# Optimization experiments

Hardware: AMD Instinct MI355X
Metric: run time of the kernel (lower is better)

## Reference

```python
import jax, jax.numpy as jnp
import numpy as np

HID = 24

def setup_inputs() -> dict:
    key = jax.random.key(0)
    ks = jax.random.split(key, 20)
    B, T = 1024, 4096
    s = 0.1
    inp = {
        "x": jax.random.normal(ks[0], (B, T, 1), jnp.float32),
        "h": jnp.zeros((3, B, HID), jnp.float32),
        # RNN layer 0 (input size 1)
        "W_ih0": jax.random.normal(ks[1], (HID, 1), jnp.float32) * s,
        "b_ih0": jax.random.normal(ks[2], (HID,), jnp.float32) * s,
        "W_hh0": jax.random.normal(ks[3], (HID, HID), jnp.float32) * s,
        "b_hh0": jax.random.normal(ks[4], (HID,), jnp.float32) * s,
        # RNN layer 1
        "W_ih1": jax.random.normal(ks[5], (HID, HID), jnp.float32) * s,
        "b_ih1": jax.random.normal(ks[6], (HID,), jnp.float32) * s,
        "W_hh1": jax.random.normal(ks[7], (HID, HID), jnp.float32) * s,
        "b_hh1": jax.random.normal(ks[8], (HID,), jnp.float32) * s,
        # RNN layer 2
        "W_ih2": jax.random.normal(ks[9], (HID, HID), jnp.float32) * s,
        "b_ih2": jax.random.normal(ks[10], (HID,), jnp.float32) * s,
        "W_hh2": jax.random.normal(ks[11], (HID, HID), jnp.float32) * s,
        "b_hh2": jax.random.normal(ks[12], (HID,), jnp.float32) * s,
        # MLP head 24 -> 24 -> 1
        "W1": jax.random.normal(ks[13], (HID, HID), jnp.float32) * s,
        "b1": jax.random.normal(ks[14], (HID,), jnp.float32) * s,
        "W2": jax.random.normal(ks[15], (1, HID), jnp.float32) * s,
        "b2": jax.random.normal(ks[16], (1,), jnp.float32) * s,
    }
    return inp


def reference(x, h,
              W_ih0, b_ih0, W_hh0, b_hh0,
              W_ih1, b_ih1, W_hh1, b_hh1,
              W_ih2, b_ih2, W_hh2, b_hh2,
              W1, b1, W2, b2):
    # x: [B, T, 1]; h: [3, B, 24]. force=True -> every step uses x[:, i, :];
    # returned y is the MLP output of the LAST timestep only.
    relu = jax.nn.relu

    def cell(carry, x_t):  # x_t: [B, 1]
        h0, h1, h2 = carry
        h0n = relu(x_t @ W_ih0.T + b_ih0 + h0 @ W_hh0.T + b_hh0)
        h1n = relu(h0n @ W_ih1.T + b_ih1 + h1 @ W_hh1.T + b_hh1)
        h2n = relu(h1n @ W_ih2.T + b_ih2 + h2 @ W_hh2.T + b_hh2)
        y = relu(relu(h2n @ W1.T + b1) @ W2.T + b2)  # [B, 1]
        return (h0n, h1n, h2n), y

    xs = jnp.swapaxes(x, 0, 1)  # [T, B, 1]
    (h0f, h1f, h2f), ys = jax.lax.scan(cell, (h[0], h[1], h[2]), xs)
    y = ys[-1]                       # [B, 1]
    h_final = jnp.stack([h0f, h1f, h2f])  # [3, B, 24]
    return y, h_final
```

## Files before the change

kernel.cpp:

```cpp
#include <hip/hip_runtime.h>

#define HID   24
#define T_LEN 4096
#define BATCH 1024
#define NB    2
#define K     32
#define NC    (T_LEN / K)
#define CTOT  (NC + 2)
#define TPB   192
#define PS    32

typedef __attribute__((ext_vector_type(2))) _Float16 h2v;
typedef __attribute__((ext_vector_type(4))) int      int4v;

#if __has_builtin(__builtin_amdgcn_fdot2)
__device__ __forceinline__ float dot2f(int p, int w, float acc) {
    return __builtin_amdgcn_fdot2(__builtin_bit_cast(h2v, p),
                                  __builtin_bit_cast(h2v, w), acc, false);
}
#else
__device__ __forceinline__ float dot2f(int p, int w, float acc) {
    h2v a = __builtin_bit_cast(h2v, p), b = __builtin_bit_cast(h2v, w);
    acc = fmaf((float)a.x, (float)b.x, acc);
    return fmaf((float)a.y, (float)b.y, acc);
}
#endif

__device__ __forceinline__ float dot4(const float4 a, const float4 b, float acc) {
    acc = fmaf(a.x, b.x, acc);
    acc = fmaf(a.y, b.y, acc);
    acc = fmaf(a.z, b.z, acc);
    return fmaf(a.w, b.w, acc);
}

#define PKF(A_, B_)                                                                 \
    (((int)__builtin_bit_cast(unsigned short, (_Float16)(B_)) << 16) |              \
     (int)__builtin_bit_cast(unsigned short, (_Float16)(A_)))

__global__ __launch_bounds__(TPB, 1) void rnn_ra_kernel(
    const float* __restrict__ x,
    const float* __restrict__ h_in,
    const float* __restrict__ Wih0, const float* __restrict__ bih0,
    const float* __restrict__ Whh0, const float* __restrict__ bhh0,
    const float* __restrict__ Wih1, const float* __restrict__ bih1,
    const float* __restrict__ Whh1, const float* __restrict__ bhh1,
    const float* __restrict__ Wih2, const float* __restrict__ bih2,
    const float* __restrict__ Whh2, const float* __restrict__ bhh2,
    const float* __restrict__ W1,   const float* __restrict__ b1,
    const float* __restrict__ W2,   const float* __restrict__ b2,
    float* __restrict__ out)
{
    __shared__ __align__(16) _Float16 row0[2][NB][PS];
    __shared__ __align__(16) _Float16 row2[2][NB][PS];
    __shared__ __align__(16) _Float16 pub1[2][NB][K][PS];
    __shared__ __align__(16) float part1[2][NB][K][PS];
    __shared__ float h2f[NB][HID];
    __shared__ float mbuf[NB][HID];

    const int tid  = threadIdx.x;
    const int l    = tid >> 6;
    const int lane = tid & 63;
    const int bl   = lane >> 5;
    const int jj   = lane & 31;
    const bool act = (jj < HID);
    const int uL   = act ? jj : (jj - 8);
    const int bg   = blockIdx.x * NB + bl;

    int4v whA, whB, whC;
    int4v wiA = {0,0,0,0}, wiB = {0,0,0,0}, wiC = {0,0,0,0};
    float wx0 = 0.f, bias;

#define MK3(ROW, DA, DB, DC) do {                                                   \
        DA = (int4v){PKF((ROW)[0], (ROW)[1]),   PKF((ROW)[2], (ROW)[3]),            \
                     PKF((ROW)[4], (ROW)[5]),   PKF((ROW)[6], (ROW)[7])};           \
        DB = (int4v){PKF((ROW)[8], (ROW)[9]),   PKF((ROW)[10], (ROW)[11]),          \
                     PKF((ROW)[12], (ROW)[13]), PKF((ROW)[14], (ROW)[15])};         \
        DC = (int4v){PKF((ROW)[16], (ROW)[17]), PKF((ROW)[18], (ROW)[19]),          \
                     PKF((ROW)[20], (ROW)[21]), PKF((ROW)[22], (ROW)[23])};         \
    } while (0)

    if (l == 0) {
        MK3(Whh0 + uL * HID, whA, whB, whC);
        MK3(Wih1 + uL * HID, wiA, wiB, wiC);
        wx0  = Wih0[uL];
        bias = bih0[uL] + bhh0[uL];
    } else if (l == 1) {
        MK3(Whh1 + uL * HID, whA, whB, whC);
        bias = bih1[uL] + bhh1[uL];
    } else {
        MK3(Whh2 + uL * HID, whA, whB, whC);
        MK3(Wih2 + uL * HID, wiA, wiB, wiC);
        bias = bih2[uL] + bhh2[uL];
    }
#undef MK3

    float cur = h_in[(l * BATCH + bg) * HID + uL];

    int4v o0, o1, o2;
    if (l == 0) {
        row0[1][bl][jj] = (_Float16)cur;
        const int4v* r = (const int4v*)&row0[1][bl][0];
        o0 = r[0]; o1 = r[1]; o2 = r[2];
    } else if (l == 1) {
        pub1[0][bl][K - 1][jj] = (_Float16)cur;
        const int4v* r = (const int4v*)&pub1[0][bl][K - 1][0];
        o0 = r[0]; o1 = r[1]; o2 = r[2];
    } else {
        row2[1][bl][jj] = (_Float16)cur;
        const int4v* r = (const int4v*)&row2[1][bl][0];
        o0 = r[0]; o1 = r[1]; o2 = r[2];
    }

    const float* xrow = x + (size_t)bg * T_LEN;
    float4 xq[8], xn[8];
    if (l == 0) {
        const float4* xr = (const float4*)xrow;
        #pragma unroll
        for (int q = 0; q < 8; ++q) xq[q] = xr[q];
    }
#define XV(S)                                                                       \
    (((S) & 3) == 0 ? xq[(S) >> 2].x : ((S) & 3) == 1 ? xq[(S) >> 2].y              \
   : ((S) & 3) == 2 ? xq[(S) >> 2].z : xq[(S) >> 2].w)

#define DOT12(V0_, V1_, V2_, W0_, W1_, W2_, A0_, A1_)                               \
    A0_ = dot2f(V0_.x, W0_.x, A0_); A1_ = dot2f(V0_.y, W0_.y, A1_);                 \
    A0_ = dot2f(V0_.z, W0_.z, A0_); A1_ = dot2f(V0_.w, W0_.w, A1_);                 \
    A0_ = dot2f(V1_.x, W1_.x, A0_); A1_ = dot2f(V1_.y, W1_.y, A1_);                 \
    A0_ = dot2f(V1_.z, W1_.z, A0_); A1_ = dot2f(V1_.w, W1_.w, A1_);                 \
    A0_ = dot2f(V2_.x, W2_.x, A0_); A1_ = dot2f(V2_.y, W2_.y, A1_);                 \
    A0_ = dot2f(V2_.z, W2_.z, A0_); A1_ = dot2f(V2_.w, W2_.w, A1_);

    __syncthreads();

    for (int c = 0; c < CTOT; ++c) {
        const int wp = c & 1, rp = wp ^ 1;
        if (l == 0) {
            if (c < NC) {
                const bool pf = (c + 1 < NC);
                if (pf) {
                    const float4* xr = (const float4*)(xrow + (size_t)(c + 1) * K);
                    #pragma unroll
                    for (int q = 0; q < 8; ++q) xn[q] = xr[q];
                }
                float* dst = &part1[wp][bl][0][0];
                #pragma unroll
                for (int s = 0; s < K; ++s) {
                    float a0 = fmaf(wx0, XV(s), bias), a1 = 0.f;
                    DOT12(o0, o1, o2, whA, whB, whC, a0, a1);
                    cur = fmaxf(a0 + a1, 0.f);
                    row0[s & 1][bl][jj] = (_Float16)cur;
                    const int4v* r = (const int4v*)&row0[s & 1][bl][0];
                    const int4v n0 = r[0], n1 = r[1], n2 = r[2];
                    if (s > 0) {
                        float p0 = 0.f, p1 = 0.f;
                        DOT12(o0, o1, o2, wiA, wiB, wiC, p0, p1);
                        dst[(s - 1) * PS + jj] = p0 + p1;
                    }
                    o0 = n0; o1 = n1; o2 = n2;
                }
                {
                    float p0 = 0.f, p1 = 0.f;
                    DOT12(o0, o1, o2, wiA, wiB, wiC, p0, p1);
                    dst[(K - 1) * PS + jj] = p0 + p1;
                }
                if (pf) {
                    #pragma unroll
                    for (int q = 0; q < 8; ++q) xq[q] = xn[q];
                }
            }
        } else if (l == 1) {
            if (c >= 1 && c < 1 + NC) {
                const float* srcp = &part1[rp][bl][0][0];
                #pragma unroll
                for (int s = 0; s < K; ++s) {
                    const float pin = srcp[s * PS + jj];
                    float a0 = pin + bias, a1 = 0.f;
                    DOT12(o0, o1, o2, whA, whB, whC, a0, a1);
                    cur = fmaxf(a0 + a1, 0.f);
                    pub1[wp][bl][s][jj] = (_Float16)cur;
                    const int4v* r = (const int4v*)&pub1[wp][bl][s][0];
                    o0 = r[0]; o1 = r[1]; o2 = r[2];
                }
            }
        } else {
            if (c >= 2 && c < 2 + NC) {
                const int4v* src = (const int4v*)&pub1[rp][bl][0][0];
                int4v iA0 = src[0], iA1 = src[1], iA2 = src[2];
                #pragma unroll
                for (int s = 0; s < K; ++s) {
                    float a0 = bias, a1 = 0.f, a2 = 0.f, a3 = 0.f;
                    DOT12(iA0, iA1, iA2, wiA, wiB, wiC, a0, a1);
                    DOT12(o0, o1, o2, whA, whB, whC, a2, a3);
                    cur = fmaxf((a0 + a1) + (a2 + a3), 0.f);
                    row2[s & 1][bl][jj] = (_Float16)cur;
                    const int4v* r = (const int4v*)&row2[s & 1][bl][0];
                    const int4v n0 = r[0], n1 = r[1], n2 = r[2];
                    if (s + 1 < K) {
                        const int4v* nr = (const int4v*)&pub1[rp][bl][s + 1][0];
                        iA0 = nr[0]; iA1 = nr[1]; iA2 = nr[2];
                    }
                    o0 = n0; o1 = n1; o2 = n2;
                }
            }
        }
        __syncthreads();
    }
#undef XV
#undef DOT12

    if (act) out[BATCH + (size_t)(l * BATCH + bg) * HID + uL] = cur;

    if (l == 2 && act) h2f[bl][uL] = cur;
    __syncthreads();
    if (l == 2 && act) {
        const float4* w1r = (const float4*)(W1 + uL * HID);
        const float4* hv  = (const float4*)&h2f[bl][0];
        float a = b1[uL];
        a = dot4(w1r[0], hv[0], a); a = dot4(w1r[1], hv[1], a);
        a = dot4(w1r[2], hv[2], a); a = dot4(w1r[3], hv[3], a);
        a = dot4(w1r[4], hv[4], a); a = dot4(w1r[5], hv[5], a);
        mbuf[bl][uL] = fmaxf(a, 0.f);
    }
    __syncthreads();
    if (l == 2 && jj == 0) {
        float a = b2[0];
        #pragma unroll
        for (int k = 0; k < HID; ++k) a = fmaf(W2[k], mbuf[bl][k], a);
        out[bg] = fmaxf(a, 0.f);
    }
}

extern "C" void kernel_launch(void* const* d_in, const int* in_sizes, int n_in,
                              void* d_out, int out_size, void* d_ws, size_t ws_size,
                              hipStream_t stream) {
    const float* x    = (const float*)d_in[0];
    const float* h_in = (const float*)d_in[1];
    const float* Wih0 = (const float*)d_in[2];
    const float* bih0 = (const float*)d_in[3];
    const float* Whh0 = (const float*)d_in[4];
    const float* bhh0 = (const float*)d_in[5];
    const float* Wih1 = (const float*)d_in[6];
    const float* bih1 = (const float*)d_in[7];
    const float* Whh1 = (const float*)d_in[8];
    const float* bhh1 = (const float*)d_in[9];
    const float* Wih2 = (const float*)d_in[10];
    const float* bih2 = (const float*)d_in[11];
    const float* Whh2 = (const float*)d_in[12];
    const float* bhh2 = (const float*)d_in[13];
    const float* W1   = (const float*)d_in[14];
    const float* b1   = (const float*)d_in[15];
    const float* W2   = (const float*)d_in[16];
    const float* b2   = (const float*)d_in[17];
    float* out = (float*)d_out;

    dim3 grid(BATCH / NB);
    dim3 block(TPB);
    hipLaunchKernelGGL(rnn_ra_kernel, grid, block, 0, stream,
                       x, h_in, Wih0, bih0, Whh0, bhh0,
                       Wih1, bih1, Whh1, bhh1, Wih2, bih2, Whh2, bhh2,
                       W1, b1, W2, b2, out);
}
```

Baseline: 510.1 us.

## Move layer-2 input projection into layer-1 wave with lagged partial sums

Layer 1's wave now computes the W_ih2 projection of its own outputs, one step behind, and writes fp32 partial sums into a new part2 buffer. Layer 2's wave then runs only its recurrent dot product plus a preloaded partial, matching how layer 0 already feeds layer 1. This balances the per-step work across the three pipelined waves and shortens layer 2's serial dependency chain. In exchange it adds shared memory for part2 and row1, and lengthens layer 1's per-step work.

```diff
diff --git a/kernel.cpp b/kernel.cpp
--- a/kernel.cpp
+++ b/kernel.cpp
@@ -37,7 +37,7 @@
     (((int)__builtin_bit_cast(unsigned short, (_Float16)(B_)) << 16) |              \
      (int)__builtin_bit_cast(unsigned short, (_Float16)(A_)))
 
-__global__ __launch_bounds__(TPB, 1) void rnn_ra_kernel(
+__global__ __launch_bounds__(TPB, 1) void rnn_lag_kernel(
     const float* __restrict__ x,
     const float* __restrict__ h_in,
     const float* __restrict__ Wih0, const float* __restrict__ bih0,
@@ -51,9 +51,10 @@
     float* __restrict__ out)
 {
     __shared__ __align__(16) _Float16 row0[2][NB][PS];
+    __shared__ __align__(16) _Float16 row1[2][NB][PS];
     __shared__ __align__(16) _Float16 row2[2][NB][PS];
-    __shared__ __align__(16) _Float16 pub1[2][NB][K][PS];
     __shared__ __align__(16) float part1[2][NB][K][PS];
+    __shared__ __align__(16) float part2[2][NB][K][PS];
     __shared__ float h2f[NB][HID];
     __shared__ float mbuf[NB][HID];
 
@@ -86,10 +87,10 @@
         bias = bih0[uL] + bhh0[uL];
     } else if (l == 1) {
         MK3(Whh1 + uL * HID, whA, whB, whC);
+        MK3(Wih2 + uL * HID, wiA, wiB, wiC);
         bias = bih1[uL] + bhh1[uL];
     } else {
         MK3(Whh2 + uL * HID, whA, whB, whC);
-        MK3(Wih2 + uL * HID, wiA, wiB, wiC);
         bias = bih2[uL] + bhh2[uL];
     }
 #undef MK3
@@ -102,8 +103,8 @@
         const int4v* r = (const int4v*)&row0[1][bl][0];
         o0 = r[0]; o1 = r[1]; o2 = r[2];
     } else if (l == 1) {
-        pub1[0][bl][K - 1][jj] = (_Float16)cur;
-        const int4v* r = (const int4v*)&pub1[0][bl][K - 1][0];
+        row1[1][bl][jj] = (_Float16)cur;
+        const int4v* r = (const int4v*)&row1[1][bl][0];
         o0 = r[0]; o1 = r[1]; o2 = r[2];
     } else {
         row2[1][bl][jj] = (_Float16)cur;
@@ -171,35 +172,41 @@
         } else if (l == 1) {
             if (c >= 1 && c < 1 + NC) {
                 const float* srcp = &part1[rp][bl][0][0];
+                float* dstp = &part2[wp][bl][0][0];
                 #pragma unroll
                 for (int s = 0; s < K; ++s) {
                     const float pin = srcp[s * PS + jj];
                     float a0 = pin + bias, a1 = 0.f;
                     DOT12(o0, o1, o2, whA, whB, whC, a0, a1);
                     cur = fmaxf(a0 + a1, 0.f);
-                    pub1[wp][bl][s][jj] = (_Float16)cur;
-                    const int4v* r = (const int4v*)&pub1[wp][bl][s][0];
-                    o0 = r[0]; o1 = r[1]; o2 = r[2];
+                    row1[s & 1][bl][jj] = (_Float16)cur;
+                    const int4v* r = (const int4v*)&row1[s & 1][bl][0];
+                    const int4v n0 = r[0], n1 = r[1], n2 = r[2];
+                    if (s > 0) {
+                        float p0 = 0.f, p1 = 0.f;
+                        DOT12(o0, o1, o2, wiA, wiB, wiC, p0, p1);
+                        dstp[(s - 1) * PS + jj] = p0 + p1;
+                    }
+                    o0 = n0; o1 = n1; o2 = n2;
+                }
+                {
+                    float p0 = 0.f, p1 = 0.f;
+                    DOT12(o0, o1, o2, wiA, wiB, wiC, p0, p1);
+                    dstp[(K - 1) * PS + jj] = p0 + p1;
                 }
             }
         } else {
             if (c >= 2 && c < 2 + NC) {
-                const int4v* src = (const int4v*)&pub1[rp][bl][0][0];
-                int4v iA0 = src[0], iA1 = src[1], iA2 = src[2];
+                const float* srcp = &part2[rp][bl][0][0];
                 #pragma unroll
                 for (int s = 0; s < K; ++s) {
-                    float a0 = bias, a1 = 0.f, a2 = 0.f, a3 = 0.f;
-                    DOT12(iA0, iA1, iA2, wiA, wiB, wiC, a0, a1);
-                    DOT12(o0, o1, o2, whA, whB, whC, a2, a3);
-                    cur = fmaxf((a0 + a1) + (a2 + a3), 0.f);
+                    const float pin = srcp[s * PS + jj];
+                    float a0 = pin + bias, a1 = 0.f;
+                    DOT12(o0, o1, o2, whA, whB, whC, a0, a1);
+                    cur = fmaxf(a0 + a1, 0.f);
                     row2[s & 1][bl][jj] = (_Float16)cur;
                     const int4v* r = (const int4v*)&row2[s & 1][bl][0];
-                    const int4v n0 = r[0], n1 = r[1], n2 = r[2];
-                    if (s + 1 < K) {
-                        const int4v* nr = (const int4v*)&pub1[rp][bl][s + 1][0];
-                        iA0 = nr[0]; iA1 = nr[1]; iA2 = nr[2];
-                    }
-                    o0 = n0; o1 = n1; o2 = n2;
+                    o0 = r[0]; o1 = r[1]; o2 = r[2];
                 }
             }
         }
@@ -255,7 +262,7 @@
 
     dim3 grid(BATCH / NB);
     dim3 block(TPB);
-    hipLaunchKernelGGL(rnn_ra_kernel, grid, block, 0, stream,
+    hipLaunchKernelGGL(rnn_lag_kernel, grid, block, 0, stream,
                        x, h_in, Wih0, bih0, Whh0, bhh0,
                        Wih1, bih1, Whh1, bhh1, Wih2, bih2, Whh2, bhh2,
                        W1, b1, W2, b2, out);
```

New measurement: 604.1 us. 1.18x slower.
